# Kernel tuning notes

Measured on AMD Instinct MI355X. Metric: run time of the kernel, lower is better.

Reference implementation:

```python
import jax, jax.numpy as jnp
import numpy as np
import math

EMBED_DIM = 1024
NUM_HEADS = 16
HEAD_DIM = EMBED_DIM // NUM_HEADS
B, S = 2, 2048


def setup_inputs() -> dict:
    key = jax.random.key(0)
    ks = jax.random.split(key, 5)
    scale = 1.0 / math.sqrt(EMBED_DIM)
    x = jax.random.normal(ks[0], (B, S, EMBED_DIM), dtype=jnp.float32)
    W_q = jax.random.normal(ks[1], (EMBED_DIM, EMBED_DIM), dtype=jnp.float32) * scale
    W_k = jax.random.normal(ks[2], (EMBED_DIM, EMBED_DIM), dtype=jnp.float32) * scale
    W_v = jax.random.normal(ks[3], (EMBED_DIM, EMBED_DIM), dtype=jnp.float32) * scale
    W_o = jax.random.normal(ks[4], (EMBED_DIM, EMBED_DIM), dtype=jnp.float32) * scale
    # causal mask: True = masked out (matches torch masked_fill semantics)
    mask = jnp.triu(jnp.ones((S, S), dtype=bool), k=1)
    return {"x": x, "mask": mask, "W_q": W_q, "W_k": W_k, "W_v": W_v, "W_o": W_o}


def _split_heads(x):
    b, s, _ = x.shape
    return x.reshape(b, s, NUM_HEADS, HEAD_DIM).transpose(0, 2, 1, 3)  # [b,h,s,hd]


def reference(x, mask, W_q, W_k, W_v, W_o):
    # torch nn.Linear(bias=False): y = x @ W.T
    Q = _split_heads(x @ W_q.T)
    K = _split_heads(x @ W_k.T)
    V = _split_heads(x @ W_v.T)
    scale = 1.0 / math.sqrt(HEAD_DIM)
    scores = jnp.einsum("bhqd,bhkd->bhqk", Q, K) * scale  # [b,h,s,s]
    scores = jnp.where(mask[None, None, :, :], -jnp.inf, scores)
    weights = jax.nn.softmax(scores, axis=-1)
    out = jnp.einsum("bhqk,bhkd->bhqd", weights, V)
    out = out.transpose(0, 2, 1, 3).reshape(x.shape[0], x.shape[1], EMBED_DIM)
    return out @ W_o.T
```

## Files before the change

kernel.cpp:

```cpp
#include <hip/hip_runtime.h>
#include <hip/hip_bf16.h>

typedef short bf16x8 __attribute__((ext_vector_type(8)));
typedef unsigned short u16x8 __attribute__((ext_vector_type(8)));
typedef unsigned short u16x4 __attribute__((ext_vector_type(4)));
typedef float f32x4 __attribute__((ext_vector_type(4)));

typedef unsigned int __attribute__((address_space(1))) gu32;
typedef unsigned int __attribute__((address_space(3))) lu32;

#define MFMA16(a, b, c) __builtin_amdgcn_mfma_f32_16x16x32_bf16((a), (b), (c), 0, 0, 0)

constexpr int SEQ = 2048;
constexpr int NH = 16;
constexpr int NTOK = 2 * SEQ;

__device__ __forceinline__ float bf2f(unsigned short u) {
  union { unsigned int i; float f; } v; v.i = ((unsigned int)u) << 16; return v.f;
}
__device__ __forceinline__ unsigned short f2bf(float f) {
  __hip_bfloat16 h = __float2bfloat16(f);
  return __builtin_bit_cast(unsigned short, h);
}
__device__ __forceinline__ unsigned int pkbf_trunc(float hi, float lo) {
  return __builtin_amdgcn_perm(__builtin_bit_cast(unsigned int, hi),
                               __builtin_bit_cast(unsigned int, lo), 0x07060302u);
}
__device__ __forceinline__ u16x8 cvt8(const float* __restrict__ p) {
  f32x4 a = *(const f32x4*)p;
  f32x4 b = *(const f32x4*)(p + 4);
  u16x8 r;
#pragma unroll
  for (int j = 0; j < 4; j++) { r[j] = f2bf(a[j]); r[4 + j] = f2bf(b[j]); }
  return r;
}

__global__ __launch_bounds__(256) void cvt_all(
    const float* __restrict__ x, const float* __restrict__ wq, const float* __restrict__ wk,
    const float* __restrict__ wv, const float* __restrict__ wo,
    unsigned short* __restrict__ Xb, unsigned short* __restrict__ Wb) {
  const int z = blockIdx.y;
  const float* src = (z == 0) ? x : (z == 1) ? wq : (z == 2) ? wk : (z == 3) ? wv : wo;
  unsigned short* dst = (z == 0) ? Xb : Wb + (size_t)(z - 1) * 1024 * 1024;
  const int n = (z == 0) ? NTOK * 1024 : 1024 * 1024;
  for (int i = (blockIdx.x * 256 + threadIdx.x) * 8; i < n; i += gridDim.x * 256 * 8)
    *(u16x8*)(dst + i) = cvt8(src + i);
}

template <int ROWS, int NWAVE>
__device__ __forceinline__ void stage_glds(const unsigned short* __restrict__ gbase,
                                           int rstride,
                                           unsigned short* __restrict__ lds,
                                           int wid, int lane) {
  constexpr int ISS = ROWS * 8 / (NWAVE * 64);
#pragma unroll
  for (int t = 0; t < ISS; ++t) {
    const int slot = (wid * ISS + t) * 64 + lane;
    const int row = slot >> 3;
    const int c8 = (slot & 7) ^ (row & 7);
    const unsigned short* gp = gbase + (size_t)row * rstride + c8 * 8;
    unsigned short* lp = lds + (size_t)(wid * ISS + t) * 512;
    __builtin_amdgcn_global_load_lds((const gu32*)gp, (lu32*)lp, 16, 0, 0);
  }
}

__device__ __forceinline__ bf16x8 frag_ld(const unsigned short* __restrict__ lds, int row, int c8) {
  const int slot = row * 8 + (c8 ^ (row & 7));
  return *(const bf16x8*)(lds + slot * 8);
}

template <int BM, int BN, int LDC, bool CF32>
__global__ __launch_bounds__(256) void gemm_lds(
    const unsigned short* __restrict__ A,
    const unsigned short* __restrict__ B,
    void* __restrict__ Cv) {
  constexpr int K = 1024;
  constexpr int MI = BM / 32, NI = BN / 32;

  __shared__ __align__(16) unsigned short As[BM * 64];
  __shared__ __align__(16) unsigned short Bs[BN * 64];

  const int tid = threadIdx.x;
  const int wid = tid >> 6;
  const int lane = tid & 63;
  const int quad = lane >> 4;
  const int c16 = lane & 15;
  const int wrow = wid >> 1, wcol = wid & 1;

  const int m0 = blockIdx.x * BM;
  const int n0 = blockIdx.y * BN;

  f32x4 acc[MI][NI];
#pragma unroll
  for (int i = 0; i < MI; i++)
#pragma unroll
    for (int j = 0; j < NI; j++) acc[i][j] = f32x4{0.f, 0.f, 0.f, 0.f};

  for (int kb = 0; kb < K; kb += 64) {
    __syncthreads();
    stage_glds<BM, 4>(A + (size_t)m0 * K + kb, K, As, wid, lane);
    stage_glds<BN, 4>(B + (size_t)n0 * K + kb, K, Bs, wid, lane);
    __syncthreads();
#pragma unroll
    for (int ks = 0; ks < 2; ++ks) {
      bf16x8 af[MI], bfr[NI];
#pragma unroll
      for (int i = 0; i < MI; i++)
        af[i] = frag_ld(As, wrow * (BM / 2) + i * 16 + c16, ks * 4 + quad);
#pragma unroll
      for (int j = 0; j < NI; j++)
        bfr[j] = frag_ld(Bs, wcol * (BN / 2) + j * 16 + c16, ks * 4 + quad);
#pragma unroll
      for (int i = 0; i < MI; i++)
#pragma unroll
        for (int j = 0; j < NI; j++) acc[i][j] = MFMA16(af[i], bfr[j], acc[i][j]);
    }
  }

#pragma unroll
  for (int i = 0; i < MI; i++) {
#pragma unroll
    for (int j = 0; j < NI; j++) {
      int row = m0 + wrow * (BM / 2) + i * 16 + quad * 4;
      int col = n0 + wcol * (BN / 2) + j * 16 + c16;
#pragma unroll
      for (int r = 0; r < 4; r++) {
        if constexpr (CF32) ((float*)Cv)[(size_t)(row + r) * LDC + col] = acc[i][j][r];
        else ((unsigned short*)Cv)[(size_t)(row + r) * LDC + col] = f2bf(acc[i][j][r]);
      }
    }
  }
}

#define SBAR do { __builtin_amdgcn_sched_barrier(0); \
                  asm volatile("s_barrier" ::: "memory"); \
                  __builtin_amdgcn_sched_barrier(0); } while (0)

__global__ __launch_bounds__(512) void gemm_8ph(
    const unsigned short* __restrict__ A,
    const unsigned short* __restrict__ B,
    unsigned short* __restrict__ C) {
  constexpr int K = 1024;
  __shared__ __align__(16) unsigned short As[2][256 * 64];
  __shared__ __align__(16) unsigned short Bs[2][256 * 64];

  const int tid = threadIdx.x;
  const int wid = tid >> 6, lane = tid & 63;
  const int quad = lane >> 4, c16 = lane & 15;
  const int wr = wid >> 2;
  const int wc = wid & 3;

  const int bid = blockIdx.x;
  const int swz = (bid & 7) * 24 + (bid >> 3);
  const int m0 = (swz / 12) * 256;
  const int n0 = (swz % 12) * 256;

  const unsigned short* Abase = A + (size_t)m0 * K;
  const unsigned short* Bbase = B + (size_t)n0 * K;

  f32x4 acc[8][4];
#pragma unroll
  for (int i = 0; i < 8; i++)
#pragma unroll
    for (int j = 0; j < 4; j++) acc[i][j] = f32x4{0.f, 0.f, 0.f, 0.f};

  bf16x8 af[4][2];
  bf16x8 bf0[2][2];
  bf16x8 bf1[2][2];

  auto lda = [&](const unsigned short* asb, int mo) {
#pragma unroll
    for (int mi = 0; mi < 4; mi++)
#pragma unroll
      for (int ks = 0; ks < 2; ks++)
        af[mi][ks] = frag_ld(asb, wr * 128 + mo + mi * 16 + c16, ks * 4 + quad);
  };
  auto ldb = [&](const unsigned short* bsb, bf16x8 (&bf)[2][2], int no) {
#pragma unroll
    for (int ni = 0; ni < 2; ni++)
#pragma unroll
      for (int ks = 0; ks < 2; ks++)
        bf[ni][ks] = frag_ld(bsb, wc * 64 + no + ni * 16 + c16, ks * 4 + quad);
  };
  auto mmq = [&](bf16x8 (&bf)[2][2], int mo, int no) {
    __builtin_amdgcn_s_setprio(1);
#pragma unroll
    for (int mi = 0; mi < 4; mi++)
#pragma unroll
      for (int ni = 0; ni < 2; ni++)
#pragma unroll
        for (int ks = 0; ks < 2; ks++)
          acc[mo + mi][no + ni] = MFMA16(af[mi][ks], bf[ni][ks], acc[mo + mi][no + ni]);
    __builtin_amdgcn_s_setprio(0);
  };

  stage_glds<128, 8>(Bbase, K, Bs[0], wid, lane);
  stage_glds<128, 8>(Bbase + (size_t)128 * K, K, Bs[0] + 8192, wid, lane);
  stage_glds<128, 8>(Abase, K, As[0], wid, lane);
  stage_glds<128, 8>(Abase + (size_t)128 * K, K, As[0] + 8192, wid, lane);
  stage_glds<128, 8>(Bbase + 64, K, Bs[1], wid, lane);
  stage_glds<128, 8>(Bbase + (size_t)128 * K + 64, K, Bs[1] + 8192, wid, lane);
  asm volatile("s_waitcnt vmcnt(4)" ::: "memory");
  SBAR;

  for (int i = 0; i < 7; ++i) {
    const int t = 2 * i;
    const int kb1 = (t + 1) * 64, kb2 = (t + 2) * 64, kb3 = (t + 3) * 64;
    lda(As[0], 0); ldb(Bs[0], bf0, 0);
    stage_glds<128, 8>(Abase + kb1, K, As[1], wid, lane);
    SBAR; mmq(bf0, 0, 0); SBAR;
    ldb(Bs[0], bf1, 32);
    stage_glds<128, 8>(Abase + (size_t)128 * K + kb1, K, As[1] + 8192, wid, lane);
    SBAR; mmq(bf1, 0, 2); SBAR;
    lda(As[0], 64);
    stage_glds<128, 8>(Bbase + kb2, K, Bs[0], wid, lane);
    SBAR; mmq(bf0, 4, 0); SBAR;
    stage_glds<128, 8>(Bbase + (size_t)128 * K + kb2, K, Bs[0] + 8192, wid, lane);
    asm volatile("s_waitcnt vmcnt(4)" ::: "memory");
    SBAR; mmq(bf1, 4, 2); SBAR;
    lda(As[1], 0); ldb(Bs[1], bf0, 0);
    stage_glds<128, 8>(Abase + kb2, K, As[0], wid, lane);
    SBAR; mmq(bf0, 0, 0); SBAR;
    ldb(Bs[1], bf1, 32);
    stage_glds<128, 8>(Abase + (size_t)128 * K + kb2, K, As[0] + 8192, wid, lane);
    SBAR; mmq(bf1, 0, 2); SBAR;
    lda(As[1], 64);
    stage_glds<128, 8>(Bbase + kb3, K, Bs[1], wid, lane);
    SBAR; mmq(bf0, 4, 0); SBAR;
    stage_glds<128, 8>(Bbase + (size_t)128 * K + kb3, K, Bs[1] + 8192, wid, lane);
    asm volatile("s_waitcnt vmcnt(4)" ::: "memory");
    SBAR; mmq(bf1, 4, 2); SBAR;
  }

  {
    const int kb1 = 15 * 64;
    lda(As[0], 0); ldb(Bs[0], bf0, 0);
    stage_glds<128, 8>(Abase + kb1, K, As[1], wid, lane);
    SBAR; mmq(bf0, 0, 0); SBAR;
    ldb(Bs[0], bf1, 32);
    stage_glds<128, 8>(Abase + (size_t)128 * K + kb1, K, As[1] + 8192, wid, lane);
    SBAR; mmq(bf1, 0, 2); SBAR;
    lda(As[0], 64);
    SBAR; mmq(bf0, 4, 0); SBAR;
    asm volatile("s_waitcnt vmcnt(0)" ::: "memory");
    SBAR; mmq(bf1, 4, 2); SBAR;
    lda(As[1], 0); ldb(Bs[1], bf0, 0);
    SBAR; mmq(bf0, 0, 0); SBAR;
    ldb(Bs[1], bf1, 32);
    SBAR; mmq(bf1, 0, 2); SBAR;
    lda(As[1], 64);
    SBAR; mmq(bf0, 4, 0); SBAR;
    SBAR; mmq(bf1, 4, 2);
  }

#pragma unroll
  for (int mi = 0; mi < 8; mi++) {
#pragma unroll
    for (int ni = 0; ni < 4; ni++) {
      const int row = m0 + wr * 128 + mi * 16 + quad * 4;
      const int col = n0 + wc * 64 + ni * 16 + c16;
#pragma unroll
      for (int r = 0; r < 4; r++)
        C[(size_t)(row + r) * 3072 + col] = f2bf(acc[mi][ni][r]);
    }
  }
}

__device__ __forceinline__ int vt_idx(int d, int kv) {
  int ck = kv >> 3;
  int s = ((d >> 3) ^ d) & 7;
  return d * 64 + ((ck ^ s) << 3) + (kv & 7);
}

struct AttnShared {
  unsigned short Kt[2][64 * 64];
  unsigned short Vt[64 * 64];
  unsigned short Pt[4][16 * 72];
};

__global__ __launch_bounds__(256) void attn_kernel(
    const unsigned short* __restrict__ QKV,
    unsigned short* __restrict__ Oa) {
  __shared__ AttnShared sh;
  const int h = blockIdx.x;
  const int b = blockIdx.y;
  const int t = 31 - blockIdx.z;
  const int tid = threadIdx.x;
  const int wid = tid >> 6, lane = tid & 63;
  const int quad = lane >> 4, c16 = lane & 15;
  const size_t tokbase = (size_t)b * SEQ;
  const int q0 = t * 64;
  const int nkv = t + 1;

  const unsigned short* qp = QKV + (tokbase + q0 + wid * 16 + c16) * 3072 + h * 64;
  bf16x8 qf[2];
#pragma unroll
  for (int ks = 0; ks < 2; ++ks) {
    u16x8 u = *(const u16x8*)(qp + ks * 32 + quad * 8);
    bf16x8 tq;
#pragma unroll
    for (int j = 0; j < 8; j++) tq[j] = (short)f2bf(0.1803368801f * bf2f(u[j]));
    qf[ks] = tq;
  }

  const unsigned short* kbase = QKV + tokbase * 3072 + 1024 + h * 64;
  const unsigned short* vbase = QKV + tokbase * 3072 + 2048 + h * 64;
  const int vkv = (tid >> 4) * 4;
  const int vd = (tid & 15) * 4;

  f32x4 o[4];
  float lacc = 0.f;
#pragma unroll
  for (int nt = 0; nt < 4; nt++) o[nt] = f32x4{0.f, 0.f, 0.f, 0.f};
  unsigned short* PtW = sh.Pt[wid];

  stage_glds<64, 4>(kbase, 3072, sh.Kt[0], wid, lane);
  u16x4 vr[4];
#pragma unroll
  for (int i = 0; i < 4; i++)
    vr[i] = *(const u16x4*)(vbase + (size_t)(vkv + i) * 3072 + vd);

  for (int kt = 0; kt < nkv; ++kt) {
    const int buf = kt & 1;
    __syncthreads();
#pragma unroll
    for (int dd = 0; dd < 4; ++dd) {
      uint2 w;
      w.x = (unsigned int)vr[0][dd] | ((unsigned int)vr[1][dd] << 16);
      w.y = (unsigned int)vr[2][dd] | ((unsigned int)vr[3][dd] << 16);
      *(uint2*)&sh.Vt[vt_idx(vd + dd, vkv)] = w;
    }
    __syncthreads();

    if (kt + 1 < nkv) {
      const size_t nofs = (size_t)(kt + 1) * 64;
      stage_glds<64, 4>(kbase + nofs * 3072, 3072, sh.Kt[buf ^ 1], wid, lane);
#pragma unroll
      for (int i = 0; i < 4; i++)
        vr[i] = *(const u16x4*)(vbase + (nofs + vkv + i) * 3072 + vd);
    }

    const unsigned short* KtB = sh.Kt[buf];
    f32x4 st[4];
#pragma unroll
    for (int nt = 0; nt < 4; ++nt) {
      f32x4 a = f32x4{-16.f, -16.f, -16.f, -16.f};
      a = MFMA16(frag_ld(KtB, nt * 16 + c16, quad), qf[0], a);
      a = MFMA16(frag_ld(KtB, nt * 16 + c16, 4 + quad), qf[1], a);
      st[nt] = a;
    }
    if (kt == nkv - 1) {
      const int kv0 = kt * 64;
      const int qg = q0 + wid * 16 + c16;
#pragma unroll
      for (int nt = 0; nt < 4; nt++)
#pragma unroll
        for (int r = 0; r < 4; r++) {
          int kg = kv0 + nt * 16 + quad * 4 + r;
          if (kg > qg) st[nt][r] = -1e30f;
        }
    }

#pragma unroll
    for (int nt = 0; nt < 4; nt++) {
      float p0 = __builtin_amdgcn_exp2f(st[nt][0]);
      float p1 = __builtin_amdgcn_exp2f(st[nt][1]);
      float p2 = __builtin_amdgcn_exp2f(st[nt][2]);
      float p3 = __builtin_amdgcn_exp2f(st[nt][3]);
      lacc += (p0 + p1) + (p2 + p3);
      uint2 w;
      w.x = pkbf_trunc(p1, p0);
      w.y = pkbf_trunc(p3, p2);
      *(uint2*)&PtW[c16 * 72 + nt * 16 + quad * 4] = w;
    }

#pragma unroll
    for (int ks = 0; ks < 2; ++ks) {
      bf16x8 pf = *(const bf16x8*)&PtW[c16 * 72 + ks * 32 + quad * 8];
#pragma unroll
      for (int nt2 = 0; nt2 < 4; ++nt2) {
        bf16x8 vf = *(const bf16x8*)&sh.Vt[vt_idx(nt2 * 16 + c16, ks * 32 + quad * 8)];
        o[nt2] = MFMA16(vf, pf, o[nt2]);
      }
    }
  }

  lacc += __shfl_xor(lacc, 16);
  lacc += __shfl_xor(lacc, 32);
  const float linv = 1.f / lacc;
  const size_t row = tokbase + q0 + wid * 16 + c16;
#pragma unroll
  for (int nt2 = 0; nt2 < 4; nt2++) {
    uint2 w;
    w.x = (unsigned int)f2bf(o[nt2][0] * linv) | ((unsigned int)f2bf(o[nt2][1] * linv) << 16);
    w.y = (unsigned int)f2bf(o[nt2][2] * linv) | ((unsigned int)f2bf(o[nt2][3] * linv) << 16);
    *(uint2*)&Oa[row * 1024 + h * 64 + nt2 * 16 + quad * 4] = w;
  }
}

template <int BM, int BN, int LDC, bool AF32, bool CF32>
__global__ __launch_bounds__(256) void gemm_bt(
    const void* __restrict__ Av, const float* __restrict__ W0, const float* __restrict__ W1,
    const float* __restrict__ W2, void* __restrict__ Cv) {
  constexpr int K = 1024;
  constexpr int LDS_LD = 72;
  constexpr int MI = BM / 32, NI = BN / 32;
  __shared__ __align__(16) unsigned short As[BM][LDS_LD];
  __shared__ __align__(16) unsigned short Bs[BN][LDS_LD];
  const int tid = threadIdx.x, wid = tid >> 6, lane = tid & 63;
  const int quad = lane >> 4, c16 = lane & 15;
  const int wrow = wid >> 1, wcol = wid & 1;
  const float* W = (blockIdx.z == 0) ? W0 : (blockIdx.z == 1 ? W1 : W2);
  const int m0 = blockIdx.y * BM, n0 = blockIdx.x * BN, cofs = blockIdx.z * 1024;
  f32x4 acc[MI][NI];
#pragma unroll
  for (int i = 0; i < MI; i++)
#pragma unroll
    for (int j = 0; j < NI; j++) acc[i][j] = f32x4{0.f, 0.f, 0.f, 0.f};
  for (int kb = 0; kb < K; kb += 64) {
    __syncthreads();
#pragma unroll
    for (int c = tid; c < BM * 8; c += 256) {
      int row = c >> 3, c8 = c & 7;
      if constexpr (AF32)
        *(u16x8*)&As[row][c8 * 8] = cvt8((const float*)Av + (size_t)(m0 + row) * K + kb + c8 * 8);
      else
        *(u16x8*)&As[row][c8 * 8] = *(const u16x8*)((const unsigned short*)Av + (size_t)(m0 + row) * K + kb + c8 * 8);
    }
#pragma unroll
    for (int c = tid; c < BN * 8; c += 256) {
      int row = c >> 3, c8 = c & 7;
      *(u16x8*)&Bs[row][c8 * 8] = cvt8(W + (size_t)(n0 + row) * K + kb + c8 * 8);
    }
    __syncthreads();
#pragma unroll
    for (int ks = 0; ks < 2; ++ks) {
      bf16x8 af[MI], bfr[NI];
#pragma unroll
      for (int i = 0; i < MI; i++)
        af[i] = *(const bf16x8*)&As[wrow * (BM / 2) + i * 16 + c16][ks * 32 + quad * 8];
#pragma unroll
      for (int j = 0; j < NI; j++)
        bfr[j] = *(const bf16x8*)&Bs[wcol * (BN / 2) + j * 16 + c16][ks * 32 + quad * 8];
#pragma unroll
      for (int i = 0; i < MI; i++)
#pragma unroll
        for (int j = 0; j < NI; j++) acc[i][j] = MFMA16(af[i], bfr[j], acc[i][j]);
    }
  }
#pragma unroll
  for (int i = 0; i < MI; i++)
#pragma unroll
    for (int j = 0; j < NI; j++) {
      int row = m0 + wrow * (BM / 2) + i * 16 + quad * 4;
      int col = n0 + wcol * (BN / 2) + j * 16 + c16 + cofs;
#pragma unroll
      for (int r = 0; r < 4; r++) {
        if constexpr (CF32) ((float*)Cv)[(size_t)(row + r) * LDC + col] = acc[i][j][r];
        else ((unsigned short*)Cv)[(size_t)(row + r) * LDC + col] = f2bf(acc[i][j][r]);
      }
    }
}

extern "C" void kernel_launch(void* const* d_in, const int* in_sizes, int n_in,
                              void* d_out, int out_size, void* d_ws, size_t ws_size,
                              hipStream_t stream) {
  const float* x = (const float*)d_in[0];
  const float* Wq = (const float*)d_in[2];
  const float* Wk = (const float*)d_in[3];
  const float* Wv = (const float*)d_in[4];
  const float* Wo = (const float*)d_in[5];
  float* out = (float*)d_out;

  unsigned short* QKV = (unsigned short*)d_ws;
  unsigned short* Wb = QKV + (size_t)NTOK * 3072;
  unsigned short* Xb = Wb + (size_t)4 * 1024 * 1024;
  unsigned short* AT = Xb;

  if (ws_size >= (size_t)40 * 1024 * 1024) {
    cvt_all<<<dim3(256, 5), 256, 0, stream>>>(x, Wq, Wk, Wv, Wo, Xb, Wb);
    gemm_8ph<<<dim3(192), 512, 0, stream>>>(Xb, Wb, QKV);
    attn_kernel<<<dim3(NH, 2, 32), 256, 0, stream>>>(QKV, AT);
    gemm_lds<128, 64, 1024, true><<<dim3(32, 16), 256, 0, stream>>>(
        AT, Wb + (size_t)3 * 1024 * 1024, out);
  } else {
    unsigned short* QKV2 = (unsigned short*)d_ws;
    unsigned short* AT2 = QKV2 + (size_t)NTOK * 3072;
    gemm_bt<128, 128, 3072, true, false><<<dim3(8, 32, 3), 256, 0, stream>>>(x, Wq, Wk, Wv, QKV2);
    attn_kernel<<<dim3(NH, 2, 32), 256, 0, stream>>>(QKV2, AT2);
    gemm_bt<64, 64, 1024, false, true><<<dim3(16, 64, 1), 256, 0, stream>>>(AT2, Wo, Wo, Wo, out);
  }
}
```

Before: 178.8 us.

## Process 128-query tiles per attention block to reuse K/V staging

Each attention block now handles two 64-row query halves (128 queries) and shares every staged K/V tile between both halves. The first half skips its MFMAs and exps once past its causal diagonal, and each half has its own diagonal masking. The grid shrinks to 16 tiles per head with a reordered tile index meant to balance the causal work. It also wraps the MFMA sections in s_setprio hints. The cost is more registers, a larger Pt buffer and half as many blocks (512), which may reduce occupancy and latency hiding.

Measured after the change: 193.3 us. +8.1%, slower.

```diff
diff --git a/kernel.cpp b/kernel.cpp
--- a/kernel.cpp
+++ b/kernel.cpp
@@ -275,7 +275,7 @@
 struct AttnShared {
   unsigned short Kt[2][64 * 64];
   unsigned short Vt[64 * 64];
-  unsigned short Pt[4][16 * 72];
+  unsigned short Pt[4][32 * 72];
 };
 
 __global__ __launch_bounds__(256) void attn_kernel(
@@ -284,23 +284,28 @@
   __shared__ AttnShared sh;
   const int h = blockIdx.x;
   const int b = blockIdx.y;
-  const int t = 31 - blockIdx.z;
+  const int zi = blockIdx.z;
+  const int T = (zi < 8) ? (15 - zi) : (zi - 8);
   const int tid = threadIdx.x;
   const int wid = tid >> 6, lane = tid & 63;
   const int quad = lane >> 4, c16 = lane & 15;
   const size_t tokbase = (size_t)b * SEQ;
-  const int q0 = t * 64;
-  const int nkv = t + 1;
-
-  const unsigned short* qp = QKV + (tokbase + q0 + wid * 16 + c16) * 3072 + h * 64;
-  bf16x8 qf[2];
-#pragma unroll
-  for (int ks = 0; ks < 2; ++ks) {
-    u16x8 u = *(const u16x8*)(qp + ks * 32 + quad * 8);
-    bf16x8 tq;
-#pragma unroll
-    for (int j = 0; j < 8; j++) tq[j] = (short)f2bf(0.1803368801f * bf2f(u[j]));
-    qf[ks] = tq;
+  const int q0 = T * 128;
+  const int nkv = 2 * T + 2;
+
+  bf16x8 qf[2][2];
+#pragma unroll
+  for (int hf = 0; hf < 2; ++hf) {
+    const unsigned short* qp =
+        QKV + (tokbase + q0 + hf * 64 + wid * 16 + c16) * 3072 + h * 64;
+#pragma unroll
+    for (int ks = 0; ks < 2; ++ks) {
+      u16x8 u = *(const u16x8*)(qp + ks * 32 + quad * 8);
+      bf16x8 tq;
+#pragma unroll
+      for (int j = 0; j < 8; j++) tq[j] = (short)f2bf(0.1803368801f * bf2f(u[j]));
+      qf[hf][ks] = tq;
+    }
   }
 
   const unsigned short* kbase = QKV + tokbase * 3072 + 1024 + h * 64;
@@ -308,10 +313,10 @@
   const int vkv = (tid >> 4) * 4;
   const int vd = (tid & 15) * 4;
 
-  f32x4 o[4];
-  float lacc = 0.f;
-#pragma unroll
-  for (int nt = 0; nt < 4; nt++) o[nt] = f32x4{0.f, 0.f, 0.f, 0.f};
+  f32x4 o0[4], o1[4];
+  float lacc0 = 0.f, lacc1 = 0.f;
+#pragma unroll
+  for (int nt = 0; nt < 4; nt++) { o0[nt] = f32x4{0.f, 0.f, 0.f, 0.f}; o1[nt] = f32x4{0.f, 0.f, 0.f, 0.f}; }
   unsigned short* PtW = sh.Pt[wid];
 
   stage_glds<64, 4>(kbase, 3072, sh.Kt[0], wid, lane);
@@ -322,6 +327,7 @@
 
   for (int kt = 0; kt < nkv; ++kt) {
     const int buf = kt & 1;
+    const bool h0act = (kt <= 2 * T);
     __syncthreads();
 #pragma unroll
     for (int dd = 0; dd < 4; ++dd) {
@@ -341,15 +347,25 @@
     }
 
     const unsigned short* KtB = sh.Kt[buf];
-    f32x4 st[4];
+    f32x4 st0[4], st1[4];
+    __builtin_amdgcn_s_setprio(1);
 #pragma unroll
     for (int nt = 0; nt < 4; ++nt) {
-      f32x4 a = f32x4{-16.f, -16.f, -16.f, -16.f};
-      a = MFMA16(frag_ld(KtB, nt * 16 + c16, quad), qf[0], a);
-      a = MFMA16(frag_ld(KtB, nt * 16 + c16, 4 + quad), qf[1], a);
-      st[nt] = a;
-    }
-    if (kt == nkv - 1) {
+      bf16x8 kfA = frag_ld(KtB, nt * 16 + c16, quad);
+      bf16x8 kfB = frag_ld(KtB, nt * 16 + c16, 4 + quad);
+      f32x4 a0 = f32x4{-16.f, -16.f, -16.f, -16.f};
+      f32x4 a1 = f32x4{-16.f, -16.f, -16.f, -16.f};
+      if (h0act) {
+        a0 = MFMA16(kfA, qf[0][0], a0);
+        a0 = MFMA16(kfB, qf[0][1], a0);
+      }
+      a1 = MFMA16(kfA, qf[1][0], a1);
+      a1 = MFMA16(kfB, qf[1][1], a1);
+      st0[nt] = a0; st1[nt] = a1;
+    }
+    __builtin_amdgcn_s_setprio(0);
+
+    if (kt == 2 * T) {
       const int kv0 = kt * 64;
       const int qg = q0 + wid * 16 + c16;
 #pragma unroll
@@ -357,44 +373,81 @@
 #pragma unroll
         for (int r = 0; r < 4; r++) {
           int kg = kv0 + nt * 16 + quad * 4 + r;
-          if (kg > qg) st[nt][r] = -1e30f;
+          if (kg > qg) st0[nt][r] = -1e30f;
         }
     }
-
+    if (kt == 2 * T + 1) {
+      const int kv0 = kt * 64;
+      const int qg = q0 + 64 + wid * 16 + c16;
+#pragma unroll
+      for (int nt = 0; nt < 4; nt++)
+#pragma unroll
+        for (int r = 0; r < 4; r++) {
+          int kg = kv0 + nt * 16 + quad * 4 + r;
+          if (kg > qg) st1[nt][r] = -1e30f;
+        }
+    }
+
+    if (h0act) {
+#pragma unroll
+      for (int nt = 0; nt < 4; nt++) {
+        float p0 = __builtin_amdgcn_exp2f(st0[nt][0]);
+        float p1 = __builtin_amdgcn_exp2f(st0[nt][1]);
+        float p2 = __builtin_amdgcn_exp2f(st0[nt][2]);
+        float p3 = __builtin_amdgcn_exp2f(st0[nt][3]);
+        lacc0 += (p0 + p1) + (p2 + p3);
+        uint2 w;
+        w.x = pkbf_trunc(p1, p0);
+        w.y = pkbf_trunc(p3, p2);
+        *(uint2*)&PtW[c16 * 72 + nt * 16 + quad * 4] = w;
+      }
+    }
 #pragma unroll
     for (int nt = 0; nt < 4; nt++) {
-      float p0 = __builtin_amdgcn_exp2f(st[nt][0]);
-      float p1 = __builtin_amdgcn_exp2f(st[nt][1]);
-      float p2 = __builtin_amdgcn_exp2f(st[nt][2]);
-      float p3 = __builtin_amdgcn_exp2f(st[nt][3]);
-      lacc += (p0 + p1) + (p2 + p3);
+      float p0 = __builtin_amdgcn_exp2f(st1[nt][0]);
+      float p1 = __builtin_amdgcn_exp2f(st1[nt][1]);
+      float p2 = __builtin_amdgcn_exp2f(st1[nt][2]);
+      float p3 = __builtin_amdgcn_exp2f(st1[nt][3]);
+      lacc1 += (p0 + p1) + (p2 + p3);
       uint2 w;
       w.x = pkbf_trunc(p1, p0);
       w.y = pkbf_trunc(p3, p2);
-      *(uint2*)&PtW[c16 * 72 + nt * 16 + quad * 4] = w;
+      *(uint2*)&PtW[(16 + c16) * 72 + nt * 16 + quad * 4] = w;
     }
 
 #pragma unroll
     for (int ks = 0; ks < 2; ++ks) {
-      bf16x8 pf = *(const bf16x8*)&PtW[c16 * 72 + ks * 32 + quad * 8];
+      bf16x8 pf0 = *(const bf16x8*)&PtW[c16 * 72 + ks * 32 + quad * 8];
+      bf16x8 pf1 = *(const bf16x8*)&PtW[(16 + c16) * 72 + ks * 32 + quad * 8];
+      __builtin_amdgcn_s_setprio(1);
 #pragma unroll
       for (int nt2 = 0; nt2 < 4; ++nt2) {
         bf16x8 vf = *(const bf16x8*)&sh.Vt[vt_idx(nt2 * 16 + c16, ks * 32 + quad * 8)];
-        o[nt2] = MFMA16(vf, pf, o[nt2]);
+        if (h0act) o0[nt2] = MFMA16(vf, pf0, o0[nt2]);
+        o1[nt2] = MFMA16(vf, pf1, o1[nt2]);
       }
-    }
-  }
-
-  lacc += __shfl_xor(lacc, 16);
-  lacc += __shfl_xor(lacc, 32);
-  const float linv = 1.f / lacc;
-  const size_t row = tokbase + q0 + wid * 16 + c16;
+      __builtin_amdgcn_s_setprio(0);
+    }
+  }
+
+  lacc0 += __shfl_xor(lacc0, 16);
+  lacc0 += __shfl_xor(lacc0, 32);
+  lacc1 += __shfl_xor(lacc1, 16);
+  lacc1 += __shfl_xor(lacc1, 32);
+  const float linv0 = 1.f / lacc0;
+  const float linv1 = 1.f / lacc1;
+  const size_t row0 = tokbase + q0 + wid * 16 + c16;
+  const size_t row1 = row0 + 64;
 #pragma unroll
   for (int nt2 = 0; nt2 < 4; nt2++) {
     uint2 w;
-    w.x = (unsigned int)f2bf(o[nt2][0] * linv) | ((unsigned int)f2bf(o[nt2][1] * linv) << 16);
-    w.y = (unsigned int)f2bf(o[nt2][2] * linv) | ((unsigned int)f2bf(o[nt2][3] * linv) << 16);
-    *(uint2*)&Oa[row * 1024 + h * 64 + nt2 * 16 + quad * 4] = w;
+    w.x = (unsigned int)f2bf(o0[nt2][0] * linv0) | ((unsigned int)f2bf(o0[nt2][1] * linv0) << 16);
+    w.y = (unsigned int)f2bf(o0[nt2][2] * linv0) | ((unsigned int)f2bf(o0[nt2][3] * linv0) << 16);
+    *(uint2*)&Oa[row0 * 1024 + h * 64 + nt2 * 16 + quad * 4] = w;
+    uint2 w1;
+    w1.x = (unsigned int)f2bf(o1[nt2][0] * linv1) | ((unsigned int)f2bf(o1[nt2][1] * linv1) << 16);
+    w1.y = (unsigned int)f2bf(o1[nt2][2] * linv1) | ((unsigned int)f2bf(o1[nt2][3] * linv1) << 16);
+    *(uint2*)&Oa[row1 * 1024 + h * 64 + nt2 * 16 + quad * 4] = w1;
   }
 }
 
@@ -480,14 +533,14 @@
   if (ws_size >= (size_t)40 * 1024 * 1024) {
     cvt_all<<<dim3(256, 5), 256, 0, stream>>>(x, Wq, Wk, Wv, Wo, Xb, Wb);
     gemm_8ph<<<dim3(192), 512, 0, stream>>>(Xb, Wb, QKV);
-    attn_kernel<<<dim3(NH, 2, 32), 256, 0, stream>>>(QKV, AT);
+    attn_kernel<<<dim3(NH, 2, 16), 256, 0, stream>>>(QKV, AT);
     gemm_lds<128, 64, 1024, true><<<dim3(32, 16), 256, 0, stream>>>(
         AT, Wb + (size_t)3 * 1024 * 1024, out);
   } else {
     unsigned short* QKV2 = (unsigned short*)d_ws;
     unsigned short* AT2 = QKV2 + (size_t)NTOK * 3072;
     gemm_bt<128, 128, 3072, true, false><<<dim3(8, 32, 3), 256, 0, stream>>>(x, Wq, Wk, Wv, QKV2);
-    attn_kernel<<<dim3(NH, 2, 32), 256, 0, stream>>>(QKV2, AT2);
+    attn_kernel<<<dim3(NH, 2, 16), 256, 0, stream>>>(QKV2, AT2);
     gemm_bt<64, 64, 1024, false, true><<<dim3(16, 64, 1), 256, 0, stream>>>(AT2, Wo, Wo, Wo, out);
   }
 }
```
